# Kernel tuning notes

Hardware: AMD Instinct MI355X
Metric: run time of the kernel (lower is better)

## Reference

```python
import jax, jax.numpy as jnp
import numpy as np

N = 20000      # num nodes
E = 320000     # num edges (avg degree 16)
F_IN = 518     # object_feature_dim
D = 128        # node_embedding_dim (= GAT out_channels)
ED = 32        # edge_embedding_dim
R = 26         # num_relations
H = 4          # GAT heads (concat=False -> mean over heads)
HID = 256      # node_encoder hidden


def _gat_layer(x, src, dst, ea, lin, lin_e, att_s, att_d, att_e, bias):
    """PyG GATConv: add_self_loops=True (fill_value='mean'), concat=False, negative_slope=0.2."""
    n = x.shape[0]
    ones = jnp.ones((src.shape[0],), x.dtype)
    cnt = jax.ops.segment_sum(ones, dst, num_segments=n)                    # [N]
    loop_ea = jax.ops.segment_sum(ea, dst, num_segments=n) / jnp.maximum(cnt, 1.0)[:, None]
    idx = jnp.arange(n)
    s = jnp.concatenate([src, idx])
    d = jnp.concatenate([dst, idx])
    ea2 = jnp.concatenate([ea, loop_ea], axis=0)                            # [E+N, ED]
    h = (x @ lin).reshape(n, H, D)                                          # [N,H,D]
    a_s = jnp.einsum('nhd,hd->nh', h, att_s)                                # [N,H]
    a_d = jnp.einsum('nhd,hd->nh', h, att_d)
    e = (ea2 @ lin_e).reshape(-1, H, D)                                     # [E+N,H,D]
    a_e = jnp.einsum('ehd,hd->eh', e, att_e)
    alpha = jax.nn.leaky_relu(a_s[s] + a_d[d] + a_e, 0.2)                   # [E+N,H]
    amax = jax.ops.segment_max(alpha, d, num_segments=n)
    alpha = jnp.exp(alpha - amax[d])
    denom = jax.ops.segment_sum(alpha, d, num_segments=n)
    alpha = alpha / (denom[d] + 1e-16)                                      # segment softmax
    msg = h[s] * alpha[:, :, None]                                          # [E+N,H,D]
    out = jax.ops.segment_sum(msg, d, num_segments=n)                       # [N,H,D]
    return out.mean(axis=1) + bias                                          # concat=False


def setup_inputs() -> dict:
    key = jax.random.key(0)
    ks = jax.random.split(key, 18)
    g = lambda k, shp, s=0.05: jax.random.normal(k, shp, jnp.float32) * s
    return {
        'x': g(ks[0], (N, F_IN), 1.0),
        'edge_index': jax.random.randint(ks[1], (2, E), 0, N),
        'edge_type': jax.random.randint(ks[2], (E,), 0, R),
        'w1': g(ks[3], (F_IN, HID)), 'b1': jnp.zeros((HID,), jnp.float32),
        'w2': g(ks[4], (HID, D)),    'b2': jnp.zeros((D,), jnp.float32),
        'rel_emb': g(ks[5], (R, ED), 1.0),
        'lin1': g(ks[6], (D, H * D)), 'line1': g(ks[7], (ED, H * D)),
        'atts1': g(ks[8], (H, D)), 'attd1': g(ks[9], (H, D)), 'atte1': g(ks[10], (H, D)),
        'bias1': jnp.zeros((D,), jnp.float32),
        'lin2': g(ks[11], (D, H * D)), 'line2': g(ks[12], (ED, H * D)),
        'atts2': g(ks[13], (H, D)), 'attd2': g(ks[14], (H, D)), 'atte2': g(ks[15], (H, D)),
        'bias2': jnp.zeros((D,), jnp.float32),
    }


def reference(x, edge_index, edge_type, w1, b1, w2, b2, rel_emb,
              lin1, line1, atts1, attd1, atte1, bias1,
              lin2, line2, atts2, attd2, atte2, bias2):
    src, dst = edge_index[0], edge_index[1]
    # node encoder (dropout inactive in eval)
    h = jax.nn.relu(x @ w1 + b1) @ w2 + b2                                  # [N,D]
    ea = rel_emb[edge_type]                                                 # [E,ED]
    h = jax.nn.relu(_gat_layer(h, src, dst, ea, lin1, line1, atts1, attd1, atte1, bias1))
    h = jax.nn.relu(_gat_layer(h, src, dst, ea, lin2, line2, atts2, attd2, atte2, bias2))
    return h
```

## Files before the change

kernel.cpp:

```cpp
#include <hip/hip_runtime.h>
#include <math.h>

#define N_NODES 20000
#define MP      20032
#define N_EDGES 320000
#define F_IN    518
#define HIDDEN  256
#define DIM     128
#define NH      4

typedef __attribute__((ext_vector_type(8))) short bf16x8;
typedef __attribute__((ext_vector_type(4))) float f32x4;
typedef unsigned short ushort_t;

__device__ __forceinline__ float lrelu02(float x) { return x > 0.f ? x : 0.2f * x; }

__device__ __forceinline__ void gl_lds16(const void* g, void* l) {
    __builtin_amdgcn_global_load_lds(
        (const __attribute__((address_space(1))) unsigned int*)g,
        (__attribute__((address_space(3))) unsigned int*)l, 16, 0, 0);
}

__device__ __forceinline__ unsigned int hi16(float v) { return __float_as_uint(v) >> 16; }
__device__ __forceinline__ unsigned int lo16(float v) {
    unsigned int h = __float_as_uint(v) & 0xFFFF0000u;
    return __float_as_uint(v - __uint_as_float(h)) >> 16;
}
__device__ __forceinline__ unsigned int rnd16(float v) {
    unsigned int u = __float_as_uint(v);
    return (u + 0x7FFFu + ((u >> 16) & 1u)) >> 16;
}
__device__ __forceinline__ float bfl(unsigned int u) { return __uint_as_float(u << 16); }
__device__ __forceinline__ float bfh(unsigned int u) { return __uint_as_float(u & 0xFFFF0000u); }

__global__ __launch_bounds__(256, 4) void gemm_mfma_v2(
    const ushort_t* __restrict__ Ah, const ushort_t* __restrict__ Al,
    const ushort_t* __restrict__ Bh, const ushort_t* __restrict__ Bl,
    const float* __restrict__ bias,
    int M, int K8, int N, int act,
    float* __restrict__ Cf,
    ushort_t* __restrict__ Ch, ushort_t* __restrict__ Cl,
    ushort_t* __restrict__ Cb,
    ushort_t* __restrict__ Ca)
{
    __shared__ __align__(16) ushort_t lds[12288];
    const int tid = threadIdx.x;
    const int w = tid >> 6, lane = tid & 63;
    const int row0 = blockIdx.y * 64, col0 = blockIdx.x * 128;
    const int nkb = K8 >> 2;
    const int m16 = lane & 15, q = lane >> 4;
    const bool use_al = (Al != nullptr);

    f32x4 acc[4][2] = {};

    for (int kb = 0; kb < nkb; ++kb) {
        const size_t kc = (size_t)(kb * 4 + w);
        const size_t aoff = (kc * MP + row0) * 8 + lane * 8;
        const size_t boff = (kc * N + col0) * 8 + lane * 8;
        gl_lds16(Ah + aoff, &lds[w * 512]);
        if (use_al) gl_lds16(Al + aoff, &lds[2048 + w * 512]);
        gl_lds16(Bh + boff,       &lds[4096 + w * 1024]);
        gl_lds16(Bh + boff + 512, &lds[4096 + w * 1024 + 512]);
        gl_lds16(Bl + boff,       &lds[8192 + w * 1024]);
        gl_lds16(Bl + boff + 512, &lds[8192 + w * 1024 + 512]);
        __syncthreads();

        bf16x8 fah[4], fal[4], fbh[2], fbl[2];
        const int fa = q * 512 + m16 * 8;
        #pragma unroll
        for (int mi = 0; mi < 4; ++mi) {
            fah[mi] = *(const bf16x8*)&lds[fa + mi * 128];
            if (use_al) fal[mi] = *(const bf16x8*)&lds[2048 + fa + mi * 128];
        }
        const int fb = q * 1024 + (w * 32 + m16) * 8;
        #pragma unroll
        for (int ni = 0; ni < 2; ++ni) {
            fbh[ni] = *(const bf16x8*)&lds[4096 + fb + ni * 128];
            fbl[ni] = *(const bf16x8*)&lds[8192 + fb + ni * 128];
        }
        #pragma unroll
        for (int mi = 0; mi < 4; ++mi)
            #pragma unroll
            for (int ni = 0; ni < 2; ++ni) {
                acc[mi][ni] = __builtin_amdgcn_mfma_f32_16x16x32_bf16(fah[mi], fbh[ni], acc[mi][ni], 0, 0, 0);
                acc[mi][ni] = __builtin_amdgcn_mfma_f32_16x16x32_bf16(fah[mi], fbl[ni], acc[mi][ni], 0, 0, 0);
            }
        if (use_al) {
            #pragma unroll
            for (int mi = 0; mi < 4; ++mi)
                #pragma unroll
                for (int ni = 0; ni < 2; ++ni)
                    acc[mi][ni] = __builtin_amdgcn_mfma_f32_16x16x32_bf16(fal[mi], fbh[ni], acc[mi][ni], 0, 0, 0);
        }
        __syncthreads();
    }

    #pragma unroll
    for (int ni = 0; ni < 2; ++ni) {
        const int col = col0 + w * 32 + ni * 16 + m16;
        const float bb = bias ? bias[col] : 0.f;
        #pragma unroll
        for (int mi = 0; mi < 4; ++mi) {
            #pragma unroll
            for (int r = 0; r < 4; ++r) {
                const int row = row0 + mi * 16 + q * 4 + r;
                if (row < M) {
                    float v = acc[mi][ni][r] + bb;
                    if (act) v = fmaxf(v, 0.f);
                    if (Cf) Cf[(size_t)row * N + col] = v;
                    if (Cb) Cb[(size_t)row * N + col] = (ushort_t)rnd16(v);
                    const size_t p = (((size_t)(col >> 3)) * MP + row) * 8 + (col & 7);
                    if (Ch) { Ch[p] = (ushort_t)hi16(v); Cl[p] = (ushort_t)lo16(v); }
                    if (Ca) Ca[p] = (ushort_t)rnd16(v);
                }
            }
        }
    }
}

__global__ __launch_bounds__(256) void conv_a_t_kernel(
    const float* __restrict__ x, ushort_t* __restrict__ xh, ushort_t* __restrict__ xl)
{
    __shared__ float tile[64][68];
    const int tid = threadIdx.x;
    const int r0 = blockIdx.x * 64;
    const int c0 = blockIdx.y * 64;

    #pragma unroll
    for (int it = 0; it < 4; ++it) {
        const int r = (tid >> 4) + it * 16;
        const int c = (tid & 15) * 4;
        const int gr = r0 + r, gc = c0 + c;
        float4 v = {0.f, 0.f, 0.f, 0.f};
        if (gr < N_NODES) {
            if (gc + 3 < F_IN) {
                v = *(const float4*)(x + (size_t)gr * F_IN + gc);
            } else {
                float tmp[4] = {0.f, 0.f, 0.f, 0.f};
                #pragma unroll
                for (int u = 0; u < 4; ++u)
                    if (gc + u < F_IN) tmp[u] = x[(size_t)gr * F_IN + gc + u];
                v.x = tmp[0]; v.y = tmp[1]; v.z = tmp[2]; v.w = tmp[3];
            }
        }
        tile[r][c] = v.x; tile[r][c+1] = v.y; tile[r][c+2] = v.z; tile[r][c+3] = v.w;
    }
    __syncthreads();

    const int k8l = tid >> 5;
    const int k8 = (c0 >> 3) + k8l;
    if (k8 >= 68) return;
    const int rr = (tid & 31) * 2;
    #pragma unroll
    for (int u = 0; u < 2; ++u) {
        const int r = rr + u;
        unsigned int hp[4], lp[4];
        #pragma unroll
        for (int i = 0; i < 4; ++i) {
            const float v0 = tile[r][k8l * 8 + 2 * i];
            const float v1 = tile[r][k8l * 8 + 2 * i + 1];
            hp[i] = (hi16(v1) << 16) | hi16(v0);
            lp[i] = (lo16(v1) << 16) | lo16(v0);
        }
        const size_t p = ((size_t)k8 * MP + r0 + r) * 8;
        *(uint4*)(xh + p) = make_uint4(hp[0], hp[1], hp[2], hp[3]);
        *(uint4*)(xl + p) = make_uint4(lp[0], lp[1], lp[2], lp[3]);
    }
}

#define W1_T (68 * 256 * 8)
#define W2_T (32 * 128 * 8)
#define L_T  (16 * 512 * 8)
__global__ __launch_bounds__(256) void conv_w_all_kernel(
    const float* __restrict__ w1, const float* __restrict__ w2,
    const float* __restrict__ l0, const float* __restrict__ l1,
    ushort_t* __restrict__ w1h, ushort_t* __restrict__ w1l,
    ushort_t* __restrict__ w2h, ushort_t* __restrict__ w2l,
    ushort_t* __restrict__ l0h, ushort_t* __restrict__ l0l,
    ushort_t* __restrict__ l1h, ushort_t* __restrict__ l1l)
{
    int idx = blockIdx.x * 256 + threadIdx.x;
    const float* w; ushort_t *bh, *bl; int K, N, local;
    if (idx < W1_T) { w = w1; bh = w1h; bl = w1l; K = F_IN; N = HIDDEN; local = idx; }
    else if (idx < W1_T + W2_T) { w = w2; bh = w2h; bl = w2l; K = HIDDEN; N = DIM; local = idx - W1_T; }
    else if (idx < W1_T + W2_T + L_T) { w = l0; bh = l0h; bl = l0l; K = DIM; N = 512; local = idx - W1_T - W2_T; }
    else if (idx < W1_T + W2_T + 2 * L_T) { w = l1; bh = l1h; bl = l1l; K = DIM; N = 512; local = idx - W1_T - W2_T - L_T; }
    else return;
    const int j = local & 7;
    const int rem = local >> 3;
    const int n = rem % N;
    const int k = (rem / N) * 8 + j;
    const float v = (k < K) ? w[(size_t)k * N + n] : 0.f;
    bh[local] = (ushort_t)hi16(v);
    bl[local] = (ushort_t)lo16(v);
}

__global__ __launch_bounds__(256) void wa2_kernel(
    const float* __restrict__ lin0, const float* __restrict__ lin1,
    const float* __restrict__ atts0, const float* __restrict__ attd0,
    const float* __restrict__ atts1, const float* __restrict__ attd1,
    float* __restrict__ wa_s0, float* __restrict__ wa_d0,
    float* __restrict__ wa_s1, float* __restrict__ wa_d1)
{
    const int wrk = blockIdx.x * 256 + threadIdx.x;
    if (wrk >= 2048) return;
    const int L = wrk >> 10;
    const int sd = (wrk >> 9) & 1;
    const int p = wrk & 511;
    const int h = p >> 7, d = p & 127;
    const float* lin = L ? lin1 : lin0;
    const float* av = L ? (sd ? attd1 : atts1) : (sd ? attd0 : atts0);
    float* out = L ? (sd ? wa_d1 : wa_s1) : (sd ? wa_d0 : wa_s0);
    const float* lp = lin + (size_t)d * (NH * DIM) + h * DIM;
    const float* ap = av + h * DIM;
    float acc = 0.f;
    #pragma unroll 8
    for (int i = 0; i < DIM; ++i) acc += lp[i] * ap[i];
    out[h * DIM + d] = acc;
}

__global__ __launch_bounds__(256) void as_ad_kernel(
    const float* __restrict__ xb, const float* __restrict__ wa_s,
    const float* __restrict__ wa_d, float* __restrict__ a_s, float* __restrict__ a_d)
{
    const int gw = blockIdx.x * 4 + (threadIdx.x >> 6);
    const int lane = threadIdx.x & 63;
    if (gw >= N_NODES * NH) return;
    const int n = gw >> 2, h = gw & 3;
    const float* hp = xb + (size_t)n * DIM;
    float2 hv = *(const float2*)(hp + lane * 2);
    float2 sv = *(const float2*)(wa_s + h * DIM + lane * 2);
    float2 dv = *(const float2*)(wa_d + h * DIM + lane * 2);
    float s = hv.x * sv.x + hv.y * sv.y;
    float d = hv.x * dv.x + hv.y * dv.y;
    #pragma unroll
    for (int off = 32; off > 0; off >>= 1) {
        s += __shfl_down(s, off);
        d += __shfl_down(d, off);
    }
    if (lane == 0) { a_s[n * 4 + h] = s; a_d[n * 4 + h] = d; }
}

__global__ __launch_bounds__(128) void rel_table2_kernel(
    const float* __restrict__ rel_emb,
    const float* __restrict__ line0, const float* __restrict__ atte0,
    const float* __restrict__ line1, const float* __restrict__ atte1,
    float* __restrict__ table)
{
    __shared__ float we[32][NH];
    const int L = blockIdx.x;
    const float* line = L ? line1 : line0;
    const float* atte = L ? atte1 : atte0;
    float* tab = table + L * 128;
    const int tid = threadIdx.x;
    const int k = tid >> 2, h = tid & 3;
    float acc = 0.f;
    for (int d = 0; d < DIM; ++d)
        acc += line[(size_t)k * (NH * DIM) + h * DIM + d] * atte[h * DIM + d];
    we[k][h] = acc;
    __syncthreads();
    if (tid < 26 * NH) {
        int r = tid >> 2, hh = tid & 3;
        float t = 0.f;
        for (int kk = 0; kk < 32; ++kk) t += rel_emb[r * 32 + kk] * we[kk][hh];
        tab[r * 4 + hh] = t;
    }
}

__global__ __launch_bounds__(256) void hist_kernel(
    const int* __restrict__ dst, int* __restrict__ cnt)
{
    const int e = blockIdx.x * blockDim.x + threadIdx.x;
    if (e >= N_EDGES) return;
    atomicAdd(&cnt[dst[e]], 1);
}

__global__ __launch_bounds__(1024) void scan_kernel(
    const int* __restrict__ cnt, int* __restrict__ ptr, int* __restrict__ ptr_copy)
{
    __shared__ int tsum[1024];
    const int tid = threadIdx.x;
    const int CH = 20;
    const int base = tid * CH;
    int s = 0;
    #pragma unroll
    for (int i = 0; i < CH; ++i) {
        int idx = base + i;
        if (idx < N_NODES) s += cnt[idx];
    }
    tsum[tid] = s;
    __syncthreads();
    for (int off = 1; off < 1024; off <<= 1) {
        int v = (tid >= off) ? tsum[tid - off] : 0;
        __syncthreads();
        tsum[tid] += v;
        __syncthreads();
    }
    int run = (tid == 0) ? 0 : tsum[tid - 1];
    #pragma unroll
    for (int i = 0; i < CH; ++i) {
        int idx = base + i;
        if (idx < N_NODES) {
            ptr[idx] = run;
            ptr_copy[idx] = run;
            run += cnt[idx];
        }
    }
    if (tid == 0) ptr[N_NODES] = N_EDGES;
}

__global__ __launch_bounds__(256) void scatter_kernel(
    const int* __restrict__ src, const int* __restrict__ dst, const int* __restrict__ etype,
    int* __restrict__ ptr_copy, int2* __restrict__ se, int* __restrict__ dcsr)
{
    const int e = blockIdx.x * blockDim.x + threadIdx.x;
    if (e >= N_EDGES) return;
    const int d = dst[e];
    const int pos = atomicAdd(&ptr_copy[d], 1);
    se[pos] = make_int2(src[e], etype[e]);
    dcsr[pos] = d;
}

__global__ __launch_bounds__(256) void edge_p_kernel(
    const int2* __restrict__ se, const int* __restrict__ dcsr,
    const float* __restrict__ a_s, const float* __restrict__ a_d,
    const float* __restrict__ table, float* __restrict__ p4)
{
    const int j0 = (blockIdx.x * 256 + threadIdx.x) * 2;
    const int2 eA = se[j0], eB = se[j0 + 1];
    const int dA = dcsr[j0], dB = dcsr[j0 + 1];
    const float4 asA = *(const float4*)(a_s + eA.x * 4);
    const float4 asB = *(const float4*)(a_s + eB.x * 4);
    const float4 adA = *(const float4*)(a_d + dA * 4);
    const float4 adB = *(const float4*)(a_d + dB * 4);
    const float4 tA  = *(const float4*)(table + eA.y * 4);
    const float4 tB  = *(const float4*)(table + eB.y * 4);
    float4 oA, oB;
    oA.x = __expf(lrelu02(asA.x + adA.x + tA.x));
    oA.y = __expf(lrelu02(asA.y + adA.y + tA.y));
    oA.z = __expf(lrelu02(asA.z + adA.z + tA.z));
    oA.w = __expf(lrelu02(asA.w + adA.w + tA.w));
    oB.x = __expf(lrelu02(asB.x + adB.x + tB.x));
    oB.y = __expf(lrelu02(asB.y + adB.y + tB.y));
    oB.z = __expf(lrelu02(asB.z + adB.z + tB.z));
    oB.w = __expf(lrelu02(asB.w + adB.w + tB.w));
    *(float4*)(p4 + (size_t)j0 * 4)     = oA;
    *(float4*)(p4 + (size_t)j0 * 4 + 4) = oB;
}

__device__ __forceinline__ void acc8(float acc[8], float p, const uint4 g)
{
    acc[0] += p * bfl(g.x); acc[1] += p * bfh(g.x);
    acc[2] += p * bfl(g.y); acc[3] += p * bfh(g.y);
    acc[4] += p * bfl(g.z); acc[5] += p * bfh(g.z);
    acc[6] += p * bfl(g.w); acc[7] += p * bfh(g.w);
}

__device__ __forceinline__ void agg_loop(
    int beg, int end, int n, int head, int cbase,
    const int2* __restrict__ se, const float* __restrict__ p4,
    const float* __restrict__ table, const float* __restrict__ a_s, float adh,
    const ushort_t* __restrict__ hb, float acc[8], float& dh)
{
    const uint4 gs = *(const uint4*)(hb + (size_t)n * 512 + cbase);

    float eh = 0.f;
    int j = beg;
    for (; j + 4 <= end; j += 4) {
        const int2 e0 = se[j],     e1 = se[j + 1];
        const int2 e2 = se[j + 2], e3 = se[j + 3];
        const float* pj = p4 + ((size_t)j * 4 + head);
        const float p0 = pj[0], p1 = pj[4], p2 = pj[8], p3 = pj[12];
        const uint4 g0 = *(const uint4*)(hb + (size_t)e0.x * 512 + cbase);
        const uint4 g1 = *(const uint4*)(hb + (size_t)e1.x * 512 + cbase);
        const uint4 g2 = *(const uint4*)(hb + (size_t)e2.x * 512 + cbase);
        const uint4 g3 = *(const uint4*)(hb + (size_t)e3.x * 512 + cbase);
        eh += (table[e0.y * 4 + head] + table[e1.y * 4 + head])
            + (table[e2.y * 4 + head] + table[e3.y * 4 + head]);
        dh += (p0 + p1) + (p2 + p3);
        acc8(acc, p0, g0); acc8(acc, p1, g1);
        acc8(acc, p2, g2); acc8(acc, p3, g3);
    }
    for (; j + 2 <= end; j += 2) {
        const int2 e0 = se[j], e1 = se[j + 1];
        const float* pj = p4 + ((size_t)j * 4 + head);
        const float p0 = pj[0], p1 = pj[4];
        const uint4 g0 = *(const uint4*)(hb + (size_t)e0.x * 512 + cbase);
        const uint4 g1 = *(const uint4*)(hb + (size_t)e1.x * 512 + cbase);
        eh += table[e0.y * 4 + head] + table[e1.y * 4 + head];
        dh += p0 + p1;
        acc8(acc, p0, g0); acc8(acc, p1, g1);
    }
    if (j < end) {
        const int2 e0 = se[j];
        const float p0 = p4[(size_t)j * 4 + head];
        const uint4 g0 = *(const uint4*)(hb + (size_t)e0.x * 512 + cbase);
        eh += table[e0.y * 4 + head];
        dh += p0;
        acc8(acc, p0, g0);
    }
    const float inv = 1.0f / fmaxf((float)(end - beg), 1.0f);
    const float ps = __expf(lrelu02(a_s[n * 4 + head] + adh + eh * inv));
    dh += ps;
    acc8(acc, ps, gs);
}

__global__ __launch_bounds__(256) void node_agg_f_kernel(
    const int* __restrict__ ptr, const int2* __restrict__ se,
    const float* __restrict__ p4, const float* __restrict__ table,
    const float* __restrict__ a_s, const float* __restrict__ a_d,
    const ushort_t* __restrict__ hb,
    const float* __restrict__ bias, ushort_t* __restrict__ oa,
    const float* __restrict__ wa_s2, const float* __restrict__ wa_d2,
    float* __restrict__ a_s2, float* __restrict__ a_d2)
{
    const int n = blockIdx.x * 4 + (threadIdx.x >> 6);
    const int lane = threadIdx.x & 63;
    if (n >= N_NODES) return;
    const int beg = ptr[n], end = ptr[n + 1];
    const int head = lane >> 4;
    const int cbase = lane * 8;
    const float adh = a_d[n * 4 + head];

    float acc[8] = {};
    float dh = 0.f;
    agg_loop(beg, end, n, head, cbase, se, p4, table, a_s, adh, hb, acc, dh);

    const float ih = 0.25f / (dh + 1e-16f);
    float t[8];
    #pragma unroll
    for (int k = 0; k < 8; ++k) {
        t[k] = acc[k] * ih;
        t[k] += __shfl_xor(t[k], 16);
        t[k] += __shfl_xor(t[k], 32);
    }
    if (lane < 16) {
        const float4 b0 = *(const float4*)(bias + cbase);
        const float4 b1 = *(const float4*)(bias + cbase + 4);
        float o[8];
        o[0] = fmaxf(t[0] + b0.x, 0.f); o[1] = fmaxf(t[1] + b0.y, 0.f);
        o[2] = fmaxf(t[2] + b0.z, 0.f); o[3] = fmaxf(t[3] + b0.w, 0.f);
        o[4] = fmaxf(t[4] + b1.x, 0.f); o[5] = fmaxf(t[5] + b1.y, 0.f);
        o[6] = fmaxf(t[6] + b1.z, 0.f); o[7] = fmaxf(t[7] + b1.w, 0.f);
        unsigned int up[4];
        #pragma unroll
        for (int i = 0; i < 4; ++i)
            up[i] = (rnd16(o[2*i+1]) << 16) | rnd16(o[2*i]);
        *(uint4*)(oa + ((size_t)lane * MP + n) * 8) = make_uint4(up[0], up[1], up[2], up[3]);
        float pss[4] = {0,0,0,0}, pdd[4] = {0,0,0,0};
        #pragma unroll
        for (int h = 0; h < NH; ++h) {
            const float* ws = wa_s2 + h * DIM + cbase;
            const float* wd = wa_d2 + h * DIM + cbase;
            #pragma unroll
            for (int i = 0; i < 8; ++i) {
                pss[h] += o[i] * ws[i];
                pdd[h] += o[i] * wd[i];
            }
        }
        #pragma unroll
        for (int m = 1; m < 16; m <<= 1) {
            #pragma unroll
            for (int h = 0; h < NH; ++h) {
                pss[h] += __shfl_xor(pss[h], m);
                pdd[h] += __shfl_xor(pdd[h], m);
            }
        }
        if (lane == 0) {
            float4 vs = {pss[0], pss[1], pss[2], pss[3]};
            float4 vd = {pdd[0], pdd[1], pdd[2], pdd[3]};
            *(float4*)(a_s2 + n * 4) = vs;
            *(float4*)(a_d2 + n * 4) = vd;
        }
    }
}

__global__ __launch_bounds__(256) void node_agg_s_kernel(
    const int* __restrict__ ptr, const int2* __restrict__ se,
    const float* __restrict__ p4, const float* __restrict__ table,
    const float* __restrict__ a_s, const float* __restrict__ a_d,
    const ushort_t* __restrict__ hb,
    const float* __restrict__ bias, float* __restrict__ outf)
{
    const int n = blockIdx.x * 4 + (threadIdx.x >> 6);
    const int lane = threadIdx.x & 63;
    if (n >= N_NODES) return;
    const int beg = ptr[n], end = ptr[n + 1];
    const int head = lane >> 4;
    const int cbase = lane * 8;
    const float adh = a_d[n * 4 + head];

    float acc[8] = {};
    float dh = 0.f;
    agg_loop(beg, end, n, head, cbase, se, p4, table, a_s, adh, hb, acc, dh);

    const float ih = 0.25f / (dh + 1e-16f);
    float t[8];
    #pragma unroll
    for (int k = 0; k < 8; ++k) {
        t[k] = acc[k] * ih;
        t[k] += __shfl_xor(t[k], 16);
        t[k] += __shfl_xor(t[k], 32);
    }
    if (lane < 16) {
        const float4 b0 = *(const float4*)(bias + cbase);
        const float4 b1 = *(const float4*)(bias + cbase + 4);
        float4 v0, v1;
        v0.x = fmaxf(t[0] + b0.x, 0.f); v0.y = fmaxf(t[1] + b0.y, 0.f);
        v0.z = fmaxf(t[2] + b0.z, 0.f); v0.w = fmaxf(t[3] + b0.w, 0.f);
        v1.x = fmaxf(t[4] + b1.x, 0.f); v1.y = fmaxf(t[5] + b1.y, 0.f);
        v1.z = fmaxf(t[6] + b1.z, 0.f); v1.w = fmaxf(t[7] + b1.w, 0.f);
        *(float4*)(outf + (size_t)n * DIM + cbase) = v0;
        *(float4*)(outf + (size_t)n * DIM + cbase + 4) = v1;
    }
}

extern "C" void kernel_launch(void* const* d_in, const int* in_sizes, int n_in,
                              void* d_out, int out_size, void* d_ws, size_t ws_size,
                              hipStream_t stream)
{
    const float* x       = (const float*)d_in[0];
    const int*   eidx    = (const int*)d_in[1];
    const int*   etype   = (const int*)d_in[2];
    const float* w1      = (const float*)d_in[3];
    const float* b1      = (const float*)d_in[4];
    const float* w2      = (const float*)d_in[5];
    const float* b2      = (const float*)d_in[6];
    const float* rel_emb = (const float*)d_in[7];
    const float* lin[2]  = {(const float*)d_in[8],  (const float*)d_in[14]};
    const float* line[2] = {(const float*)d_in[9],  (const float*)d_in[15]};
    const float* atts[2] = {(const float*)d_in[10], (const float*)d_in[16]};
    const float* attd[2] = {(const float*)d_in[11], (const float*)d_in[17]};
    const float* atte[2] = {(const float*)d_in[12], (const float*)d_in[18]};
    const float* bias[2] = {(const float*)d_in[13], (const float*)d_in[19]};
    const int* src = eidx;
    const int* dst = eidx + N_EDGES;

    char* base = (char*)d_ws;
    size_t off = 0;
    auto alloc = [&](size_t bytes) -> void* {
        void* p = base + off;
        off = (off + bytes + 255) & ~(size_t)255;
        return p;
    };
    ushort_t* xh  = (ushort_t*)alloc((size_t)68 * MP * 8 * 2);
    ushort_t* xl  = (ushort_t*)alloc((size_t)68 * MP * 8 * 2);
    ushort_t* h1h = (ushort_t*)alloc((size_t)32 * MP * 8 * 2);
    ushort_t* h1l = (ushort_t*)alloc((size_t)32 * MP * 8 * 2);
    ushort_t* x0a = (ushort_t*)alloc((size_t)16 * MP * 8 * 2);
    void* reg1    = alloc((size_t)16 * MP * 8 * 4);
    ushort_t* w1h = (ushort_t*)alloc(W1_T * 2);
    ushort_t* w1l = (ushort_t*)alloc(W1_T * 2);
    ushort_t* w2h = (ushort_t*)alloc(W2_T * 2);
    ushort_t* w2l = (ushort_t*)alloc(W2_T * 2);
    ushort_t* l0h = (ushort_t*)alloc(L_T * 2);
    ushort_t* l0l = (ushort_t*)alloc(L_T * 2);
    ushort_t* l1h = (ushort_t*)alloc(L_T * 2);
    ushort_t* l1l = (ushort_t*)alloc(L_T * 2);
    float* a_s0  = (float*)alloc(N_NODES * 4 * 4);
    float* a_d0  = (float*)alloc(N_NODES * 4 * 4);
    float* a_s1  = (float*)alloc(N_NODES * 4 * 4);
    float* a_d1  = (float*)alloc(N_NODES * 4 * 4);
    float* table = (float*)alloc(2 * 128 * 4);
    float* wa_s0 = (float*)alloc(512 * 4);
    float* wa_d0 = (float*)alloc(512 * 4);
    float* wa_s1 = (float*)alloc(512 * 4);
    float* wa_d1 = (float*)alloc(512 * 4);
    int*  cnt_i  = (int*)alloc(N_NODES * 4);
    int*  ptr    = (int*)alloc((N_NODES + 4) * 4);
    int*  ptrc   = (int*)alloc(N_NODES * 4);
    int2* se     = (int2*)alloc((size_t)N_EDGES * 8);
    int*  dcsr   = (int*)alloc((size_t)N_EDGES * 4);
    float* p4    = (float*)alloc((size_t)N_EDGES * 4 * 4);

    ushort_t* hb = xh;
    float* xbuf0 = (float*)reg1;
    ushort_t* x1a = (ushort_t*)reg1;

    const int mtiles = MP / 64;
    const int ep_grid = N_EDGES / 512;

    conv_a_t_kernel<<<dim3(MP / 64, 9), 256, 0, stream>>>(x, xh, xl);
    conv_w_all_kernel<<<(W1_T + W2_T + 2 * L_T + 255) / 256, 256, 0, stream>>>(
        w1, w2, lin[0], lin[1], w1h, w1l, w2h, w2l, l0h, l0l, l1h, l1l);
    wa2_kernel<<<8, 256, 0, stream>>>(lin[0], lin[1], atts[0], attd[0], atts[1], attd[1],
                                      wa_s0, wa_d0, wa_s1, wa_d1);
    rel_table2_kernel<<<2, 128, 0, stream>>>(rel_emb, line[0], atte[0], line[1], atte[1], table);

    hipMemsetAsync(cnt_i, 0, N_NODES * sizeof(int), stream);
    hist_kernel<<<(N_EDGES + 255) / 256, 256, 0, stream>>>(dst, cnt_i);
    scan_kernel<<<1, 1024, 0, stream>>>(cnt_i, ptr, ptrc);
    scatter_kernel<<<(N_EDGES + 255) / 256, 256, 0, stream>>>(src, dst, etype, ptrc, se, dcsr);

    gemm_mfma_v2<<<dim3(HIDDEN / 128, mtiles), 256, 0, stream>>>(
        xh, xl, w1h, w1l, b1, N_NODES, 68, HIDDEN, 1, nullptr, h1h, h1l, nullptr, nullptr);
    gemm_mfma_v2<<<dim3(DIM / 128, mtiles), 256, 0, stream>>>(
        h1h, h1l, w2h, w2l, b2, N_NODES, 32, DIM, 0, xbuf0, nullptr, nullptr, nullptr, x0a);

    gemm_mfma_v2<<<dim3((NH * DIM) / 128, mtiles), 256, 0, stream>>>(
        x0a, nullptr, l0h, l0l, nullptr, N_NODES, 16, NH * DIM, 0, nullptr, nullptr, nullptr, hb, nullptr);
    as_ad_kernel<<<N_NODES, 256, 0, stream>>>(xbuf0, wa_s0, wa_d0, a_s0, a_d0);
    edge_p_kernel<<<ep_grid, 256, 0, stream>>>(se, dcsr, a_s0, a_d0, table, p4);
    node_agg_f_kernel<<<(N_NODES + 3) / 4, 256, 0, stream>>>(
        ptr, se, p4, table, a_s0, a_d0, hb, bias[0], x1a,
        wa_s1, wa_d1, a_s1, a_d1);

    gemm_mfma_v2<<<dim3((NH * DIM) / 128, mtiles), 256, 0, stream>>>(
        x1a, nullptr, l1h, l1l, nullptr, N_NODES, 16, NH * DIM, 0, nullptr, nullptr, nullptr, hb, nullptr);
    edge_p_kernel<<<ep_grid, 256, 0, stream>>>(se, dcsr, a_s1, a_d1, table + 128, p4);
    node_agg_s_kernel<<<(N_NODES + 3) / 4, 256, 0, stream>>>(
        ptr, se, p4, table + 128, a_s1, a_d1, hb, bias[1], (float*)d_out);
}
```

Measured before the change: 419.0 us.

## Fuse two-layer node encoder MLP into one MFMA kernel keeping hidden in LDS

Replaces the two encoder GEMM launches with a single kernel. Each block computes a 64-row tile of relu(x@W1+b1) in registers, writes it as hi/lo bf16 split into LDS, and immediately multiplies by W2. This removes the write and re-read of the 256-wide hidden activation and one launch. The cost is that each block now covers all 256 hidden columns, so there are fewer blocks (313 vs 626 before). It also carries higher register pressure from a 4x4 accumulator array, with launch bounds requesting 3 waves per SIMD.

Measured after the change: 412.9 us. Within noise of the previous version (-1.4%).

```diff
diff --git a/kernel.cpp b/kernel.cpp
--- a/kernel.cpp
+++ b/kernel.cpp
@@ -112,6 +112,132 @@
                     const size_t p = (((size_t)(col >> 3)) * MP + row) * 8 + (col & 7);
                     if (Ch) { Ch[p] = (ushort_t)hi16(v); Cl[p] = (ushort_t)lo16(v); }
                     if (Ca) Ca[p] = (ushort_t)rnd16(v);
+                }
+            }
+        }
+    }
+}
+
+__global__ __launch_bounds__(256, 3) void enc_fused_kernel(
+    const ushort_t* __restrict__ Ah, const ushort_t* __restrict__ Al,
+    const ushort_t* __restrict__ B1h, const ushort_t* __restrict__ B1l,
+    const ushort_t* __restrict__ B2h, const ushort_t* __restrict__ B2l,
+    const float* __restrict__ b1, const float* __restrict__ b2,
+    float* __restrict__ Cf, ushort_t* __restrict__ Ca)
+{
+    __shared__ __align__(16) ushort_t lds[24576];
+    const int tid = threadIdx.x;
+    const int w = tid >> 6, lane = tid & 63;
+    const int row0 = blockIdx.x * 64;
+    const int m16 = lane & 15, q = lane >> 4;
+
+    f32x4 acc1[4][4] = {};
+    for (int kb = 0; kb < 17; ++kb) {
+        const size_t kc = (size_t)(kb * 4 + w);
+        const size_t aoff = (kc * MP + row0) * 8 + lane * 8;
+        const size_t boff = kc * 2048 + lane * 8;
+        gl_lds16(Ah + aoff, &lds[w * 512]);
+        gl_lds16(Al + aoff, &lds[2048 + w * 512]);
+        #pragma unroll
+        for (int u = 0; u < 4; ++u) {
+            gl_lds16(B1h + boff + u * 512, &lds[4096 + w * 2048 + u * 512]);
+            gl_lds16(B1l + boff + u * 512, &lds[12288 + w * 2048 + u * 512]);
+        }
+        __syncthreads();
+
+        bf16x8 fah[4], fal[4], fbh[4], fbl[4];
+        const int fa = q * 512 + m16 * 8;
+        #pragma unroll
+        for (int mi = 0; mi < 4; ++mi) {
+            fah[mi] = *(const bf16x8*)&lds[fa + mi * 128];
+            fal[mi] = *(const bf16x8*)&lds[2048 + fa + mi * 128];
+        }
+        #pragma unroll
+        for (int ni = 0; ni < 4; ++ni) {
+            const int fb = q * 2048 + (ni * 64 + w * 16 + m16) * 8;
+            fbh[ni] = *(const bf16x8*)&lds[4096 + fb];
+            fbl[ni] = *(const bf16x8*)&lds[12288 + fb];
+        }
+        #pragma unroll
+        for (int mi = 0; mi < 4; ++mi)
+            #pragma unroll
+            for (int ni = 0; ni < 4; ++ni) {
+                acc1[mi][ni] = __builtin_amdgcn_mfma_f32_16x16x32_bf16(fah[mi], fbh[ni], acc1[mi][ni], 0, 0, 0);
+                acc1[mi][ni] = __builtin_amdgcn_mfma_f32_16x16x32_bf16(fah[mi], fbl[ni], acc1[mi][ni], 0, 0, 0);
+                acc1[mi][ni] = __builtin_amdgcn_mfma_f32_16x16x32_bf16(fal[mi], fbh[ni], acc1[mi][ni], 0, 0, 0);
+            }
+        __syncthreads();
+    }
+
+    float b1c[4];
+    #pragma unroll
+    for (int ni = 0; ni < 4; ++ni) b1c[ni] = b1[ni * 64 + w * 16 + m16];
+
+    f32x4 acc2[4][2] = {};
+    const int kc2l = w * 2 + (m16 >> 3);
+    const int k7 = m16 & 7;
+    for (int st = 0; st < 4; ++st) {
+        #pragma unroll
+        for (int mi = 0; mi < 4; ++mi)
+            #pragma unroll
+            for (int r = 0; r < 4; ++r) {
+                const float v = fmaxf(acc1[mi][st][r] + b1c[st], 0.f);
+                const int ad = kc2l * 512 + (mi * 16 + q * 4 + r) * 8 + k7;
+                lds[ad] = (ushort_t)hi16(v);
+                lds[4096 + ad] = (ushort_t)lo16(v);
+            }
+        #pragma unroll
+        for (int c = 0; c < 2; ++c) {
+            const size_t bo = (size_t)(st * 8 + w * 2 + c) * 1024 + lane * 8;
+            const int dl = (w * 2 + c) * 1024;
+            gl_lds16(B2h + bo,       &lds[8192 + dl]);
+            gl_lds16(B2h + bo + 512, &lds[8192 + dl + 512]);
+            gl_lds16(B2l + bo,       &lds[16384 + dl]);
+            gl_lds16(B2l + bo + 512, &lds[16384 + dl + 512]);
+        }
+        __syncthreads();
+
+        #pragma unroll
+        for (int kb2 = 0; kb2 < 2; ++kb2) {
+            bf16x8 ah[4], al[4], bh[2], bl[2];
+            const int fa2 = (kb2 * 4 + q) * 512 + m16 * 8;
+            #pragma unroll
+            for (int mi = 0; mi < 4; ++mi) {
+                ah[mi] = *(const bf16x8*)&lds[fa2 + mi * 128];
+                al[mi] = *(const bf16x8*)&lds[4096 + fa2 + mi * 128];
+            }
+            #pragma unroll
+            for (int ni = 0; ni < 2; ++ni) {
+                const int fb2 = (kb2 * 4 + q) * 1024 + (w * 32 + ni * 16 + m16) * 8;
+                bh[ni] = *(const bf16x8*)&lds[8192 + fb2];
+                bl[ni] = *(const bf16x8*)&lds[16384 + fb2];
+            }
+            #pragma unroll
+            for (int mi = 0; mi < 4; ++mi)
+                #pragma unroll
+                for (int ni = 0; ni < 2; ++ni) {
+                    acc2[mi][ni] = __builtin_amdgcn_mfma_f32_16x16x32_bf16(ah[mi], bh[ni], acc2[mi][ni], 0, 0, 0);
+                    acc2[mi][ni] = __builtin_amdgcn_mfma_f32_16x16x32_bf16(ah[mi], bl[ni], acc2[mi][ni], 0, 0, 0);
+                    acc2[mi][ni] = __builtin_amdgcn_mfma_f32_16x16x32_bf16(al[mi], bh[ni], acc2[mi][ni], 0, 0, 0);
+                }
+        }
+        __syncthreads();
+    }
+
+    #pragma unroll
+    for (int ni = 0; ni < 2; ++ni) {
+        const int col = w * 32 + ni * 16 + m16;
+        const float bb = b2[col];
+        #pragma unroll
+        for (int mi = 0; mi < 4; ++mi) {
+            #pragma unroll
+            for (int r = 0; r < 4; ++r) {
+                const int row = row0 + mi * 16 + q * 4 + r;
+                if (row < N_NODES) {
+                    const float v = acc2[mi][ni][r] + bb;
+                    Cf[(size_t)row * DIM + col] = v;
+                    const size_t p = (((size_t)(col >> 3)) * MP + row) * 8 + (col & 7);
+                    Ca[p] = (ushort_t)rnd16(v);
                 }
             }
         }
@@ -545,8 +671,6 @@
     };
     ushort_t* xh  = (ushort_t*)alloc((size_t)68 * MP * 8 * 2);
     ushort_t* xl  = (ushort_t*)alloc((size_t)68 * MP * 8 * 2);
-    ushort_t* h1h = (ushort_t*)alloc((size_t)32 * MP * 8 * 2);
-    ushort_t* h1l = (ushort_t*)alloc((size_t)32 * MP * 8 * 2);
     ushort_t* x0a = (ushort_t*)alloc((size_t)16 * MP * 8 * 2);
     void* reg1    = alloc((size_t)16 * MP * 8 * 4);
     ushort_t* w1h = (ushort_t*)alloc(W1_T * 2);
@@ -592,10 +716,8 @@
     scan_kernel<<<1, 1024, 0, stream>>>(cnt_i, ptr, ptrc);
     scatter_kernel<<<(N_EDGES + 255) / 256, 256, 0, stream>>>(src, dst, etype, ptrc, se, dcsr);
 
-    gemm_mfma_v2<<<dim3(HIDDEN / 128, mtiles), 256, 0, stream>>>(
-        xh, xl, w1h, w1l, b1, N_NODES, 68, HIDDEN, 1, nullptr, h1h, h1l, nullptr, nullptr);
-    gemm_mfma_v2<<<dim3(DIM / 128, mtiles), 256, 0, stream>>>(
-        h1h, h1l, w2h, w2l, b2, N_NODES, 32, DIM, 0, xbuf0, nullptr, nullptr, nullptr, x0a);
+    enc_fused_kernel<<<mtiles, 256, 0, stream>>>(
+        xh, xl, w1h, w1l, w2h, w2l, b1, b2, xbuf0, x0a);
 
     gemm_mfma_v2<<<dim3((NH * DIM) / 128, mtiles), 256, 0, stream>>>(
         x0a, nullptr, l0h, l0l, nullptr, N_NODES, 16, NH * DIM, 0, nullptr, nullptr, nullptr, hb, nullptr);
```
